# Optimization experiments

Measured on AMD Instinct MI355X. Metric: run time of the kernel, lower is better.

Reference implementation:

```python
import jax, jax.numpy as jnp
import numpy as np

N = 100000
E = 1600000
D_IN = 128
D_H = 128


def setup_inputs() -> dict:
    key = jax.random.key(0)
    ks = jax.random.split(key, 6)
    x = jax.random.normal(ks[0], (N, D_IN), dtype=jnp.float32)
    edge_index = jax.random.randint(ks[1], (2, E), 0, N, dtype=jnp.int64)
    s1 = 1.0 / np.sqrt(D_IN)
    s2 = 1.0 / np.sqrt(D_H)
    W1l = jax.random.normal(ks[2], (D_IN, D_H), dtype=jnp.float32) * s1
    W1r = jax.random.normal(ks[3], (D_IN, D_H), dtype=jnp.float32) * s1
    W2l = jax.random.normal(ks[4], (D_H, D_H), dtype=jnp.float32) * s2
    W2r = jax.random.normal(ks[5], (D_H, D_H), dtype=jnp.float32) * s2
    b1 = jnp.zeros((D_H,), dtype=jnp.float32)
    b2 = jnp.zeros((D_H,), dtype=jnp.float32)
    return {"x": x, "edge_index": edge_index, "W1l": W1l, "b1": b1,
            "W1r": W1r, "W2l": W2l, "b2": b2, "W2r": W2r}


def _sage_conv(x, src, dst, Wl, b, Wr):
    # mean-aggregate neighbor features: messages flow src -> dst
    agg = jax.ops.segment_sum(x[src], dst, num_segments=N)  # [N, d]
    deg = jax.ops.segment_sum(jnp.ones((src.shape[0],), x.dtype), dst,
                              num_segments=N)
    mean = agg / jnp.maximum(deg, 1.0)[:, None]
    # PyG SAGEConv: lin_l(aggr) + lin_r(x); bias lives in lin_l
    return mean @ Wl + b + x @ Wr


def reference(x, edge_index, W1l, b1, W1r, W2l, b2, W2r):
    src, dst = edge_index[0], edge_index[1]
    h = jax.nn.relu(_sage_conv(x, src, dst, W1l, b1, W1r))
    return _sage_conv(h, src, dst, W2l, b2, W2r)
```

## Files before the change

### kernel.cpp

```cpp
#include <hip/hip_runtime.h>


typedef __attribute__((ext_vector_type(8))) short short8;
typedef __attribute__((ext_vector_type(4))) float floatx4;
typedef __attribute__((ext_vector_type(4))) unsigned short ushort4v;

#define BSH1 9
#define CHUNK 2048

__device__ inline unsigned short f2b(float f) {
    unsigned u = __builtin_bit_cast(unsigned, f);
    return (unsigned short)((u + 0x7FFFu + ((u >> 16) & 1u)) >> 16);
}
__device__ inline float blo(unsigned v) { return __builtin_bit_cast(float, v << 16); }
__device__ inline float bhi(unsigned v) { return __builtin_bit_cast(float, v & 0xffff0000u); }

__global__ void detect_kernel(const int* __restrict__ e32, int nelem, int* flag) {
    __shared__ int bad;
    if (threadIdx.x == 0) bad = 0;
    __syncthreads();
    int half = nelem >> 1;
    int viol = 0;
    for (int i = threadIdx.x; i < 4096; i += blockDim.x) {
        long long k = ((long long)i * half) / 4096;
        if (e32[2 * k + 1] != 0) viol++;
    }
    if (viol) atomicAdd(&bad, viol);
    __syncthreads();
    if (threadIdx.x == 0) flag[0] = (bad == 0) ? 1 : 0;
}

__device__ inline void decode_edge(const int* e32, bool is64, int E, int i, int& s, int& d) {
    if (is64) { s = e32[2 * (long long)i]; d = e32[2 * ((long long)E + i)]; }
    else      { s = e32[i];                d = e32[E + i]; }
}

__global__ __launch_bounds__(256) void coarse_count_kernel(const int* __restrict__ e32,
                                                           const int* __restrict__ flag,
                                                           int* __restrict__ bcnt,
                                                           int E, int nb1) {
    extern __shared__ int lh[];
    for (int i = threadIdx.x; i < nb1; i += blockDim.x) lh[i] = 0;
    __syncthreads();
    bool is64 = flag[0] != 0;
    int stride = gridDim.x * blockDim.x;
    for (int i = blockIdx.x * blockDim.x + threadIdx.x; i < E; i += stride) {
        int d = is64 ? e32[2 * ((long long)E + i)] : e32[E + i];
        atomicAdd(&lh[d >> BSH1], 1);
    }
    __syncthreads();
    for (int i = threadIdx.x; i < nb1; i += blockDim.x) {
        int c = lh[i];
        if (c) atomicAdd(&bcnt[i], c);
    }
}

__global__ __launch_bounds__(1024) void scan_kernel(const int* __restrict__ deg,
                                                    int* __restrict__ off,
                                                    int* __restrict__ cursor, int N) {
    __shared__ int wsum[16];
    __shared__ int s_carry;
    int t = threadIdx.x;
    int lane = t & 63, w = t >> 6;
    if (t == 0) s_carry = 0;
    __syncthreads();
    for (int base = 0; base < N; base += 1024) {
        int i = base + t;
        int v = (i < N) ? deg[i] : 0;
        int sc = v;
        #pragma unroll
        for (int o = 1; o < 64; o <<= 1) {
            int u = __shfl_up(sc, o, 64);
            if (lane >= o) sc += u;
        }
        if (lane == 63) wsum[w] = sc;
        __syncthreads();
        int woff = 0;
        for (int j = 0; j < w; ++j) woff += wsum[j];
        int c = s_carry;
        int excl = c + woff + (sc - v);
        if (i < N) { off[i] = excl; cursor[i] = excl; }
        __syncthreads();
        if (t == 1023) s_carry = c + woff + sc;
        __syncthreads();
    }
    if (t == 0) off[N] = s_carry;
}

__global__ __launch_bounds__(256) void coarse_scatter_kernel(const int* __restrict__ e32,
                                                             const int* __restrict__ flag,
                                                             int* __restrict__ bcur,
                                                             unsigned* __restrict__ pairs,
                                                             int E, int nb1) {
    extern __shared__ int lh[];
    int t = threadIdx.x;
    bool is64 = flag[0] != 0;
    int nchunks = (E + CHUNK - 1) / CHUNK;
    for (int ch = blockIdx.x; ch < nchunks; ch += gridDim.x) {
        int e0 = ch * CHUNK;
        int e1 = min(e0 + CHUNK, E);
        for (int i = t; i < nb1; i += 256) lh[i] = 0;
        __syncthreads();
        int dreg[CHUNK / 256];
        #pragma unroll
        for (int j = 0; j < CHUNK / 256; ++j) {
            int i = e0 + j * 256 + t;
            int d = -1;
            if (i < e1) d = is64 ? e32[2 * ((long long)E + i)] : e32[E + i];
            dreg[j] = d;
            if (d >= 0) atomicAdd(&lh[d >> BSH1], 1);
        }
        __syncthreads();
        for (int i = t; i < nb1; i += 256) {
            int c = lh[i];
            lh[nb1 + i] = c ? atomicAdd(&bcur[i], c) : 0;
            lh[i] = 0;
        }
        __syncthreads();
        #pragma unroll
        for (int j = 0; j < CHUNK / 256; ++j) {
            int i = e0 + j * 256 + t;
            if (i < e1) {
                int s = is64 ? e32[2 * (long long)i] : e32[i];
                int d = dreg[j];
                int k = d >> BSH1;
                int r = atomicAdd(&lh[k], 1);
                pairs[lh[nb1 + k] + r] = (unsigned)s | ((unsigned)(d & ((1 << BSH1) - 1)) << 23);
            }
        }
        __syncthreads();
    }
}

__global__ __launch_bounds__(256) void fine_csr_kernel(const unsigned* __restrict__ pairs,
                                                       const int* __restrict__ boff,
                                                       int* __restrict__ off,
                                                       int* __restrict__ csr,
                                                       int N, int nb1, int E) {
    __shared__ int ldeg[512], loff[512];
    __shared__ int wsum[4];
    int b = blockIdx.x;
    if (b >= nb1) return;
    int t = threadIdx.x;
    int p0 = boff[b], p1 = boff[b + 1];
    int base = b << BSH1;
    ldeg[2 * t] = 0; ldeg[2 * t + 1] = 0;
    __syncthreads();
    for (int i = p0 + t; i < p1; i += 256) atomicAdd(&ldeg[pairs[i] >> 23], 1);
    __syncthreads();
    {
        int lane = t & 63, w = t >> 6;
        int v0 = ldeg[2 * t], v1 = ldeg[2 * t + 1];
        int v = v0 + v1, sc = v;
        #pragma unroll
        for (int o = 1; o < 64; o <<= 1) {
            int u = __shfl_up(sc, o, 64);
            if (lane >= o) sc += u;
        }
        if (lane == 63) wsum[w] = sc;
        __syncthreads();
        int cross = 0;
        for (int j = 0; j < w; ++j) cross += wsum[j];
        int ex = cross + sc - v;
        loff[2 * t] = ex;
        loff[2 * t + 1] = ex + v0;
        int d0 = base + 2 * t, d1 = d0 + 1;
        if (d0 < N) off[d0] = p0 + ex;
        if (d1 < N) off[d1] = p0 + ex + v0;
    }
    __syncthreads();
    ldeg[2 * t] = 0; ldeg[2 * t + 1] = 0;
    __syncthreads();
    for (int i = p0 + t; i < p1; i += 256) {
        unsigned e = pairs[i];
        int dl = e >> 23;
        int r = atomicAdd(&ldeg[dl], 1);
        csr[p0 + loff[dl] + r] = (int)(e & 0x7FFFFFu);
    }
    if (b == 0 && t == 0) off[N] = E;
}

__global__ void cvt_kernel(const float* __restrict__ in, unsigned short* __restrict__ out, int n4) {
    int stride = gridDim.x * blockDim.x;
    for (int i = blockIdx.x * blockDim.x + threadIdx.x; i < n4; i += stride) {
        float4 v = ((const float4*)in)[i];
        ushort4v o;
        o[0] = f2b(v.x); o[1] = f2b(v.y); o[2] = f2b(v.z); o[3] = f2b(v.w);
        ((ushort4v*)out)[i] = o;
    }
}

template<int BF16IN>
__global__ __launch_bounds__(256) void spmm_mean_kernel(const void* __restrict__ Xv,
                                                        const int* __restrict__ off,
                                                        const int* __restrict__ csr,
                                                        unsigned* __restrict__ outb, int N) {
    int wid = blockIdx.x * 4 + (threadIdx.x >> 6);
    int lane = threadIdx.x & 63;
    if (wid >= N) return;
    int b0 = off[wid], b1 = off[wid + 1];
    float ax = 0.f, ay = 0.f;
    int i = b0;
    if (BF16IN) {
        const unsigned* X = (const unsigned*)Xv;
        for (; i + 7 < b1; i += 8) {
            int s0 = csr[i],     s1 = csr[i + 1], s2 = csr[i + 2], s3 = csr[i + 3];
            int s4 = csr[i + 4], s5 = csr[i + 5], s6 = csr[i + 6], s7 = csr[i + 7];
            unsigned v0 = X[(long long)s0 * 64 + lane];
            unsigned v1 = X[(long long)s1 * 64 + lane];
            unsigned v2 = X[(long long)s2 * 64 + lane];
            unsigned v3 = X[(long long)s3 * 64 + lane];
            unsigned v4 = X[(long long)s4 * 64 + lane];
            unsigned v5 = X[(long long)s5 * 64 + lane];
            unsigned v6 = X[(long long)s6 * 64 + lane];
            unsigned v7 = X[(long long)s7 * 64 + lane];
            ax += (blo(v0) + blo(v1)) + (blo(v2) + blo(v3)) +
                  ((blo(v4) + blo(v5)) + (blo(v6) + blo(v7)));
            ay += (bhi(v0) + bhi(v1)) + (bhi(v2) + bhi(v3)) +
                  ((bhi(v4) + bhi(v5)) + (bhi(v6) + bhi(v7)));
        }
        for (; i + 3 < b1; i += 4) {
            int s0 = csr[i], s1 = csr[i + 1], s2 = csr[i + 2], s3 = csr[i + 3];
            unsigned v0 = X[(long long)s0 * 64 + lane];
            unsigned v1 = X[(long long)s1 * 64 + lane];
            unsigned v2 = X[(long long)s2 * 64 + lane];
            unsigned v3 = X[(long long)s3 * 64 + lane];
            ax += blo(v0) + blo(v1) + blo(v2) + blo(v3);
            ay += bhi(v0) + bhi(v1) + bhi(v2) + bhi(v3);
        }
        for (; i < b1; ++i) {
            unsigned v = X[(long long)csr[i] * 64 + lane];
            ax += blo(v); ay += bhi(v);
        }
    } else {
        const float2* X = (const float2*)Xv;
        for (; i + 3 < b1; i += 4) {
            int s0 = csr[i], s1 = csr[i + 1], s2 = csr[i + 2], s3 = csr[i + 3];
            float2 v0 = X[(long long)s0 * 64 + lane];
            float2 v1 = X[(long long)s1 * 64 + lane];
            float2 v2 = X[(long long)s2 * 64 + lane];
            float2 v3 = X[(long long)s3 * 64 + lane];
            ax += v0.x + v1.x + v2.x + v3.x;
            ay += v0.y + v1.y + v2.y + v3.y;
        }
        for (; i < b1; ++i) {
            float2 v = X[(long long)csr[i] * 64 + lane];
            ax += v.x; ay += v.y;
        }
    }
    int dgr = b1 - b0;
    float inv = (dgr > 0) ? 1.0f / (float)dgr : 0.0f;
    unsigned pack = (unsigned)f2b(ax * inv) | ((unsigned)f2b(ay * inv) << 16);
    outb[(long long)wid * 64 + lane] = pack;
}

#define WT_SZ   (128 * 264)
#define APANEL  (64 * 136)
#define ABUF    (2 * APANEL)
#define GEMM_LDS ((WT_SZ + 2 * ABUF) * 2)

template<int XF32, int OUTMODE>
__global__ __launch_bounds__(512, 1) void gemm_mfma_kernel(
    const unsigned short* __restrict__ Am, const void* __restrict__ Ax,
    const float* __restrict__ Wl, const float* __restrict__ Wr,
    const float* __restrict__ bias, void* __restrict__ Out,
    int N, int ntiles)
{
    extern __shared__ unsigned short lds[];
    unsigned short* Wt = lds;
    int t = threadIdx.x;
    int lane = t & 63, wv = t >> 6;
    int lm = lane & 15, q = lane >> 4;
    int c0 = wv * 16;

    for (int it = 0; it < 32; ++it) {
        int n = t & 127;
        int kp = it * 4 + (t >> 7);
        int k = 2 * kp;
        const float* Wsrc = (k < 128) ? (Wl + k * 128) : (Wr + (k - 128) * 128);
        unsigned pack = (unsigned)f2b(Wsrc[n]) | ((unsigned)f2b(Wsrc[128 + n]) << 16);
        *(unsigned*)(Wt + n * 264 + k) = pack;
    }

    float bias0 = bias[c0 + lm];

    short8 pm[2], px[2];
    auto prefetch = [&](int tl) {
        long long row0 = (long long)tl * 64;
        #pragma unroll
        for (int j = 0; j < 2; ++j) {
            int cid = j * 512 + t;
            int row = cid >> 4, cp = cid & 15;
            long long gr = row0 + row;
            bool ok = gr < (long long)N;
            pm[j] = ok ? *(const short8*)(Am + gr * 128 + cp * 8) : (short8)0;
            if (XF32) {
                short8 s = (short8)0;
                if (ok) {
                    const float* xp = (const float*)Ax + gr * 128 + cp * 8;
                    floatx4 u0 = *(const floatx4*)xp;
                    floatx4 u1 = *(const floatx4*)(xp + 4);
                    s[0] = (short)f2b(u0[0]); s[1] = (short)f2b(u0[1]);
                    s[2] = (short)f2b(u0[2]); s[3] = (short)f2b(u0[3]);
                    s[4] = (short)f2b(u1[0]); s[5] = (short)f2b(u1[1]);
                    s[6] = (short)f2b(u1[2]); s[7] = (short)f2b(u1[3]);
                }
                px[j] = s;
            } else {
                px[j] = ok ? *(const short8*)((const unsigned short*)Ax + gr * 128 + cp * 8)
                           : (short8)0;
            }
        }
    };

    int tile = blockIdx.x;
    if (tile < ntiles) prefetch(tile);
    int buf = 0;
    for (; tile < ntiles; tile += gridDim.x) {
        unsigned short* A = lds + WT_SZ + buf * ABUF;
        __syncthreads();
        #pragma unroll
        for (int j = 0; j < 2; ++j) {
            int cid = j * 512 + t;
            int row = cid >> 4, cp = cid & 15;
            *(short8*)(A + row * 136 + cp * 8) = pm[j];
            *(short8*)(A + APANEL + row * 136 + cp * 8) = px[j];
        }
        __syncthreads();
        int nt = tile + gridDim.x;
        if (nt < ntiles) prefetch(nt);

        floatx4 acc[4];
        #pragma unroll
        for (int rf = 0; rf < 4; ++rf) acc[rf] = (floatx4)bias0;
        #pragma unroll
        for (int ks = 0; ks < 8; ++ks) {
            const unsigned short* P = A + (ks >= 4 ? APANEL : 0);
            int k0 = (ks & 3) * 32 + q * 8;
            short8 b0 = *(const short8*)(Wt + (c0 + lm) * 264 + ks * 32 + q * 8);
            #pragma unroll
            for (int rf = 0; rf < 4; ++rf) {
                short8 a = *(const short8*)(P + (rf * 16 + lm) * 136 + k0);
                acc[rf] = __builtin_amdgcn_mfma_f32_16x16x32_bf16(a, b0, acc[rf], 0, 0, 0);
            }
        }

        long long r0 = (long long)tile * 64;
        int col = c0 + lm;
        #pragma unroll
        for (int rf = 0; rf < 4; ++rf) {
            #pragma unroll
            for (int rg = 0; rg < 4; ++rg) {
                long long rr = r0 + rf * 16 + q * 4 + rg;
                if (rr < (long long)N) {
                    float v = acc[rf][rg];
                    if (OUTMODE != 2) v = fmaxf(v, 0.f);
                    if (OUTMODE == 1)
                        ((unsigned short*)Out)[rr * 128 + col] = f2b(v);
                    else
                        ((float*)Out)[rr * 128 + col] = v;
                }
            }
        }
        buf ^= 1;
    }
}

extern "C" void kernel_launch(void* const* d_in, const int* in_sizes, int n_in,
                              void* d_out, int out_size, void* d_ws, size_t ws_size,
                              hipStream_t stream) {
    const float* x   = (const float*)d_in[0];
    const int*   eix = (const int*)d_in[1];
    const float* W1l = (const float*)d_in[2];
    const float* b1  = (const float*)d_in[3];
    const float* W1r = (const float*)d_in[4];
    const float* W2l = (const float*)d_in[5];
    const float* b2  = (const float*)d_in[6];
    const float* W2r = (const float*)d_in[7];
    float* out = (float*)d_out;

    int N = in_sizes[0] / 128;
    int E = in_sizes[1] / 2;
    if (N <= 0 || E <= 0) return;
    int nb1 = (N + (1 << BSH1) - 1) >> BSH1;

    char* ws = (char*)d_ws;
    size_t o = 0;
    auto alloc = [&](size_t bytes) -> void* {
        o = (o + 255) & ~(size_t)255;
        void* p = ws + o;
        o += bytes;
        return p;
    };
    int*            flag   = (int*)alloc(4);
    int*            bcnt   = (int*)alloc((size_t)nb1 * 4);
    int*            boff   = (int*)alloc(((size_t)nb1 + 1) * 4);
    int*            bcur   = (int*)alloc((size_t)nb1 * 4);
    int*            off    = (int*)alloc(((size_t)N + 1) * 4);
    int*            csr    = (int*)alloc((size_t)E * 4);
    unsigned short* xb     = (unsigned short*)alloc((size_t)N * 128 * 2);
    unsigned short* meanb  = (unsigned short*)alloc((size_t)N * 128 * 2);
    unsigned short* hb     = (unsigned short*)alloc((size_t)N * 128 * 2);
    bool full = (o <= ws_size);
    unsigned* pairs = (unsigned*)meanb;

    (void)hipFuncSetAttribute((const void*)gemm_mfma_kernel<0, 0>,
                              hipFuncAttributeMaxDynamicSharedMemorySize, GEMM_LDS);
    (void)hipFuncSetAttribute((const void*)gemm_mfma_kernel<0, 1>,
                              hipFuncAttributeMaxDynamicSharedMemorySize, GEMM_LDS);
    (void)hipFuncSetAttribute((const void*)gemm_mfma_kernel<0, 2>,
                              hipFuncAttributeMaxDynamicSharedMemorySize, GEMM_LDS);
    (void)hipFuncSetAttribute((const void*)gemm_mfma_kernel<1, 2>,
                              hipFuncAttributeMaxDynamicSharedMemorySize, GEMM_LDS);

    hipMemsetAsync(bcnt, 0, (size_t)nb1 * 4, stream);

    detect_kernel<<<1, 256, 0, stream>>>(eix, in_sizes[1], flag);
    size_t cnt_lds = (size_t)nb1 * 4;
    coarse_count_kernel<<<256, 256, cnt_lds, stream>>>(eix, flag, bcnt, E, nb1);
    scan_kernel<<<1, 1024, 0, stream>>>(bcnt, boff, bcur, nb1);
    int nchunks = (E + CHUNK - 1) / CHUNK;
    int sgrid = nchunks < 2048 ? nchunks : 2048;
    coarse_scatter_kernel<<<sgrid, 256, 2 * cnt_lds, stream>>>(eix, flag, bcur, pairs, E, nb1);
    fine_csr_kernel<<<nb1, 256, 0, stream>>>(pairs, boff, off, csr, N, nb1, E);

    cvt_kernel<<<2048, 256, 0, stream>>>(x, xb, N * 32);

    int spmm_grid = (N + 3) / 4;
    int ntiles = (N + 63) / 64;
    int ggrid = ntiles < 256 ? ntiles : 256;

    spmm_mean_kernel<1><<<spmm_grid, 256, 0, stream>>>(xb, off, csr, (unsigned*)meanb, N);
    if (full) {
        gemm_mfma_kernel<0, 1><<<ggrid, 512, GEMM_LDS, stream>>>(
            meanb, xb, W1l, W1r, b1, hb, N, ntiles);
        spmm_mean_kernel<1><<<spmm_grid, 256, 0, stream>>>(hb, off, csr, (unsigned*)meanb, N);
        gemm_mfma_kernel<0, 2><<<ggrid, 512, GEMM_LDS, stream>>>(
            meanb, hb, W2l, W2r, b2, out, N, ntiles);
    } else {
        gemm_mfma_kernel<0, 0><<<ggrid, 512, GEMM_LDS, stream>>>(
            meanb, xb, W1l, W1r, b1, out, N, ntiles);
        spmm_mean_kernel<0><<<spmm_grid, 256, 0, stream>>>(out, off, csr, (unsigned*)meanb, N);
        gemm_mfma_kernel<1, 2><<<ggrid, 512, GEMM_LDS, stream>>>(
            meanb, out, W2l, W2r, b2, out, N, ntiles);
    }
}
```

Before: 262.1 us.

## Fuse bf16 cast into edge count kernel; hold GEMM weights in registers

The x-to-bf16 conversion is merged into the coarse edge-count kernel as extra blocks, so one launch is removed and the two independent jobs overlap. In the GEMM, each wave now loads its weight fragments from LDS into registers once, and the LDS is then reused only for double-buffered A panels. That shrinks the shared-memory footprint, which allows a launch bound of 4 blocks per CU and a grid of 512 blocks instead of 256. The cost is higher register pressure from the 8 short8 weight fragments, and LDS is still needed temporarily at kernel start to stage the weights.

```diff
diff --git a/kernel.cpp b/kernel.cpp
--- a/kernel.cpp
+++ b/kernel.cpp
@@ -35,23 +35,36 @@
     else      { s = e32[i];                d = e32[E + i]; }
 }
 
-__global__ __launch_bounds__(256) void coarse_count_kernel(const int* __restrict__ e32,
-                                                           const int* __restrict__ flag,
-                                                           int* __restrict__ bcnt,
-                                                           int E, int nb1) {
-    extern __shared__ int lh[];
-    for (int i = threadIdx.x; i < nb1; i += blockDim.x) lh[i] = 0;
-    __syncthreads();
-    bool is64 = flag[0] != 0;
-    int stride = gridDim.x * blockDim.x;
-    for (int i = blockIdx.x * blockDim.x + threadIdx.x; i < E; i += stride) {
-        int d = is64 ? e32[2 * ((long long)E + i)] : e32[E + i];
-        atomicAdd(&lh[d >> BSH1], 1);
-    }
-    __syncthreads();
-    for (int i = threadIdx.x; i < nb1; i += blockDim.x) {
-        int c = lh[i];
-        if (c) atomicAdd(&bcnt[i], c);
+__global__ __launch_bounds__(256) void cvt_count_kernel(const float* __restrict__ xin,
+                                                        unsigned short* __restrict__ xb, int n4,
+                                                        const int* __restrict__ e32,
+                                                        const int* __restrict__ flag,
+                                                        int* __restrict__ bcnt,
+                                                        int E, int nb1, int cvtB) {
+    if ((int)blockIdx.x < cvtB) {
+        int stride = cvtB * 256;
+        for (int i = blockIdx.x * 256 + threadIdx.x; i < n4; i += stride) {
+            float4 v = ((const float4*)xin)[i];
+            ushort4v o;
+            o[0] = f2b(v.x); o[1] = f2b(v.y); o[2] = f2b(v.z); o[3] = f2b(v.w);
+            ((ushort4v*)xb)[i] = o;
+        }
+    } else {
+        extern __shared__ int lh[];
+        for (int i = threadIdx.x; i < nb1; i += 256) lh[i] = 0;
+        __syncthreads();
+        bool is64 = flag[0] != 0;
+        int cb = gridDim.x - cvtB;
+        int stride = cb * 256;
+        for (int i = (blockIdx.x - cvtB) * 256 + threadIdx.x; i < E; i += stride) {
+            int d = is64 ? e32[2 * ((long long)E + i)] : e32[E + i];
+            atomicAdd(&lh[d >> BSH1], 1);
+        }
+        __syncthreads();
+        for (int i = threadIdx.x; i < nb1; i += 256) {
+            int c = lh[i];
+            if (c) atomicAdd(&bcnt[i], c);
+        }
     }
 }
 
@@ -178,16 +191,6 @@
         csr[p0 + loff[dl] + r] = (int)(e & 0x7FFFFFu);
     }
     if (b == 0 && t == 0) off[N] = E;
-}
-
-__global__ void cvt_kernel(const float* __restrict__ in, unsigned short* __restrict__ out, int n4) {
-    int stride = gridDim.x * blockDim.x;
-    for (int i = blockIdx.x * blockDim.x + threadIdx.x; i < n4; i += stride) {
-        float4 v = ((const float4*)in)[i];
-        ushort4v o;
-        o[0] = f2b(v.x); o[1] = f2b(v.y); o[2] = f2b(v.z); o[3] = f2b(v.w);
-        ((ushort4v*)out)[i] = o;
-    }
 }
 
 template<int BF16IN>
@@ -254,20 +257,21 @@
     outb[(long long)wid * 64 + lane] = pack;
 }
 
-#define WT_SZ   (128 * 264)
-#define APANEL  (64 * 136)
-#define ABUF    (2 * APANEL)
-#define GEMM_LDS ((WT_SZ + 2 * ABUF) * 2)
+#define APAD       136
+#define WT_STRIDE  264
+#define WT_SHORTS  (128 * WT_STRIDE)
+#define APANEL2    (64 * APAD)
+#define ABUF2      (2 * APANEL2)
+#define GEMM_LDS   (2 * ABUF2 * 2)
 
 template<int XF32, int OUTMODE>
-__global__ __launch_bounds__(512, 1) void gemm_mfma_kernel(
+__global__ __launch_bounds__(512, 4) void gemm_mfma_kernel(
     const unsigned short* __restrict__ Am, const void* __restrict__ Ax,
     const float* __restrict__ Wl, const float* __restrict__ Wr,
     const float* __restrict__ bias, void* __restrict__ Out,
     int N, int ntiles)
 {
     extern __shared__ unsigned short lds[];
-    unsigned short* Wt = lds;
     int t = threadIdx.x;
     int lane = t & 63, wv = t >> 6;
     int lm = lane & 15, q = lane >> 4;
@@ -279,8 +283,14 @@
         int k = 2 * kp;
         const float* Wsrc = (k < 128) ? (Wl + k * 128) : (Wr + (k - 128) * 128);
         unsigned pack = (unsigned)f2b(Wsrc[n]) | ((unsigned)f2b(Wsrc[128 + n]) << 16);
-        *(unsigned*)(Wt + n * 264 + k) = pack;
-    }
+        *(unsigned*)(lds + n * WT_STRIDE + k) = pack;
+    }
+    __syncthreads();
+    short8 breg[8];
+    #pragma unroll
+    for (int ks = 0; ks < 8; ++ks)
+        breg[ks] = *(const short8*)(lds + (c0 + lm) * WT_STRIDE + ks * 32 + q * 8);
+    __syncthreads();
 
     float bias0 = bias[c0 + lm];
 
@@ -317,14 +327,14 @@
     if (tile < ntiles) prefetch(tile);
     int buf = 0;
     for (; tile < ntiles; tile += gridDim.x) {
-        unsigned short* A = lds + WT_SZ + buf * ABUF;
+        unsigned short* A = lds + buf * ABUF2;
         __syncthreads();
         #pragma unroll
         for (int j = 0; j < 2; ++j) {
             int cid = j * 512 + t;
             int row = cid >> 4, cp = cid & 15;
-            *(short8*)(A + row * 136 + cp * 8) = pm[j];
-            *(short8*)(A + APANEL + row * 136 + cp * 8) = px[j];
+            *(short8*)(A + row * APAD + cp * 8) = pm[j];
+            *(short8*)(A + APANEL2 + row * APAD + cp * 8) = px[j];
         }
         __syncthreads();
         int nt = tile + gridDim.x;
@@ -335,13 +345,12 @@
         for (int rf = 0; rf < 4; ++rf) acc[rf] = (floatx4)bias0;
         #pragma unroll
         for (int ks = 0; ks < 8; ++ks) {
-            const unsigned short* P = A + (ks >= 4 ? APANEL : 0);
+            const unsigned short* P = A + (ks >= 4 ? APANEL2 : 0);
             int k0 = (ks & 3) * 32 + q * 8;
-            short8 b0 = *(const short8*)(Wt + (c0 + lm) * 264 + ks * 32 + q * 8);
             #pragma unroll
             for (int rf = 0; rf < 4; ++rf) {
-                short8 a = *(const short8*)(P + (rf * 16 + lm) * 136 + k0);
-                acc[rf] = __builtin_amdgcn_mfma_f32_16x16x32_bf16(a, b0, acc[rf], 0, 0, 0);
+                short8 a = *(const short8*)(P + (rf * 16 + lm) * APAD + k0);
+                acc[rf] = __builtin_amdgcn_mfma_f32_16x16x32_bf16(a, breg[ks], acc[rf], 0, 0, 0);
             }
         }
 
@@ -417,18 +426,17 @@
 
     detect_kernel<<<1, 256, 0, stream>>>(eix, in_sizes[1], flag);
     size_t cnt_lds = (size_t)nb1 * 4;
-    coarse_count_kernel<<<256, 256, cnt_lds, stream>>>(eix, flag, bcnt, E, nb1);
+    cvt_count_kernel<<<2048 + 256, 256, cnt_lds, stream>>>(x, xb, N * 32,
+                                                           eix, flag, bcnt, E, nb1, 2048);
     scan_kernel<<<1, 1024, 0, stream>>>(bcnt, boff, bcur, nb1);
     int nchunks = (E + CHUNK - 1) / CHUNK;
     int sgrid = nchunks < 2048 ? nchunks : 2048;
     coarse_scatter_kernel<<<sgrid, 256, 2 * cnt_lds, stream>>>(eix, flag, bcur, pairs, E, nb1);
     fine_csr_kernel<<<nb1, 256, 0, stream>>>(pairs, boff, off, csr, N, nb1, E);
 
-    cvt_kernel<<<2048, 256, 0, stream>>>(x, xb, N * 32);
-
     int spmm_grid = (N + 3) / 4;
     int ntiles = (N + 63) / 64;
-    int ggrid = ntiles < 256 ? ntiles : 256;
+    int ggrid = ntiles < 512 ? ntiles : 512;
 
     spmm_mean_kernel<1><<<spmm_grid, 256, 0, stream>>>(xb, off, csr, (unsigned*)meanb, N);
     if (full) {
```

Result: faster. 255.7 us (-2.4%).
